# Kernel optimization log

Measured on AMD Instinct MI355X. Metric: run time of the kernel, lower is better.

Reference implementation:

```python
import jax, jax.numpy as jnp
import numpy as np

HEADS = 16
DIM_HEAD = 64
MAX_REL_POS = 16  # temporal_length


def setup_inputs() -> dict:
    key = jax.random.key(0)
    ks = jax.random.split(key, 8)
    B, T, D = 2048, 16, 1024
    inner = HEADS * DIM_HEAD  # 1024
    w = 0.02  # weight init scale for numerical stability
    return {
        "x": jax.random.normal(ks[0], (B, T, D), jnp.float32),
        "Wq": jax.random.normal(ks[1], (inner, D), jnp.float32) * w,
        "Wk": jax.random.normal(ks[2], (inner, D), jnp.float32) * w,
        "Wv": jax.random.normal(ks[3], (inner, D), jnp.float32) * w,
        "Wo": jax.random.normal(ks[4], (D, inner), jnp.float32) * w,
        "bo": jnp.zeros((D,), jnp.float32),
        "rel_k_table": jax.random.normal(ks[5], (2 * MAX_REL_POS + 1, DIM_HEAD), jnp.float32) * w,
        "rel_v_table": jax.random.normal(ks[6], (2 * MAX_REL_POS + 1, DIM_HEAD), jnp.float32) * w,
    }


def reference(x, Wq, Wk, Wv, Wo, bo, rel_k_table, rel_v_table):
    B, T, D = x.shape
    h, dh = HEADS, DIM_HEAD
    scale = dh ** -0.5

    def split_heads(t):  # [B,T,h*dh] -> [B*h,T,dh]
        return t.reshape(B, T, h, dh).transpose(0, 2, 1, 3).reshape(B * h, T, dh)

    q = split_heads(x @ Wq.T)
    k = split_heads(x @ Wk.T)
    v = split_heads(x @ Wv.T)

    sim = jnp.einsum('bid,bjd->bij', q, k) * scale

    # relative-position bias: idx[i,j] = clip(j-i, -L, L) + L
    r = jnp.arange(T)
    idx = jnp.clip(r[None, :] - r[:, None], -MAX_REL_POS, MAX_REL_POS) + MAX_REL_POS
    k2 = rel_k_table[idx]  # [T,T,dh]
    sim = sim + jnp.einsum('btd,tsd->bts', q, k2) * scale

    attn = jax.nn.softmax(sim, axis=-1)
    out = jnp.einsum('bij,bjd->bid', attn, v)
    v2 = rel_v_table[idx]  # [T,T,dh]
    out = out + jnp.einsum('bts,tsd->btd', attn, v2)

    out = out.reshape(B, h, T, dh).transpose(0, 2, 1, 3).reshape(B, T, h * dh)
    return out @ Wo.T + bo
```

## Files before the change

### kernel.cpp

```cpp
#include <hip/hip_runtime.h>

#define HEADS 16
#define DIM_HEAD 64
#define T_SEQ 16
#define D_MODEL 1024
#define MAX_REL 16

typedef _Float16 half8 __attribute__((ext_vector_type(8)));
typedef float f32x4 __attribute__((ext_vector_type(4)));

__global__ __launch_bounds__(256)
void cvt_f32_f16(const float* __restrict__ in, _Float16* __restrict__ out, int n8) {
  int i = blockIdx.x * blockDim.x + threadIdx.x;
  if (i >= n8) return;
  float4 a = ((const float4*)in)[2 * i];
  float4 b = ((const float4*)in)[2 * i + 1];
  half8 h;
  h[0] = (_Float16)a.x; h[1] = (_Float16)a.y;
  h[2] = (_Float16)a.z; h[3] = (_Float16)a.w;
  h[4] = (_Float16)b.x; h[5] = (_Float16)b.y;
  h[6] = (_Float16)b.z; h[7] = (_Float16)b.w;
  ((half8*)out)[i] = h;
}

__device__ __forceinline__ void gload_lds16(const _Float16* g, _Float16* l) {
  __builtin_amdgcn_global_load_lds(
      (const __attribute__((address_space(1))) unsigned int*)(uintptr_t)g,
      (__attribute__((address_space(3))) unsigned int*)(uintptr_t)l, 16, 0, 0);
}

template <bool OUT_F16>
__global__ __launch_bounds__(512, 2)
void gemm256(const _Float16* __restrict__ A, const _Float16* __restrict__ B,
             const float* __restrict__ bias, void* __restrict__ Cv,
             int M, int N, int K) {
  __shared__ _Float16 lds[2][2][2][128][64];
  const int tid = threadIdx.x;
  const int wave = tid >> 6, lane = tid & 63;
  const int wm = wave >> 2, wn = wave & 3;
  const int bm = blockIdx.y, bn = blockIdx.x;
  const int fr = lane & 15;
  const int q4 = lane >> 4;
  const int l3 = lane >> 3;
  const int sl = (lane & 7) ^ l3;

  const _Float16* Ag = A + (size_t)(bm * 256) * K;
  const _Float16* Bg = B + (size_t)(bn * 256) * K;

  f32x4 acc[8][4];
#pragma unroll
  for (int m = 0; m < 8; ++m)
#pragma unroll
    for (int n = 0; n < 4; ++n) acc[m][n] = (f32x4){0.f, 0.f, 0.f, 0.f};

  auto stage_half = [&](int buf, int ab, int half, const _Float16* G, int k0) {
#pragma unroll
    for (int i = 0; i < 2; ++i) {
      int g = wave * 2 + i;
      const _Float16* src =
          G + (size_t)(half * 128 + g * 8 + l3) * K + k0 + sl * 8;
      gload_lds16(src, &lds[buf][ab][half][g * 8][0]);
    }
  };

  auto ldA = [&](int buf, int mf, int ks) {
    unsigned off = (unsigned)((mf * 16 + fr) * 128 + (ks * 4 + q4) * 16) ^
                   (unsigned)((fr & 7) << 4);
    return *(const half8*)((const char*)&lds[buf][0][wm][0][0] + off);
  };
  auto ldB = [&](int buf, int nf, int ks) {
    int rowB = wn * 64 + nf * 16 + fr;
    unsigned off = (unsigned)((rowB & 127) * 128 + (ks * 4 + q4) * 16) ^
                   (unsigned)((fr & 7) << 4);
    return *(const half8*)((const char*)&lds[buf][1][rowB >> 7][0][0] + off);
  };

#pragma unroll
  for (int h = 0; h < 2; ++h) {
    stage_half(0, 0, h, Ag, 0);
    stage_half(0, 1, h, Bg, 0);
  }
  asm volatile("s_waitcnt vmcnt(0)" ::: "memory");
  __builtin_amdgcn_s_barrier();

  const int NT = K >> 6;
  for (int t = 0; t < NT; ++t) {
    const int cur = t & 1, nxt = cur ^ 1;
    const bool pf = (t + 1 < NT);
    const int k1 = (t + 1) << 6;
    half8 bF[4][2];
#pragma unroll
    for (int p = 0; p < 4; ++p) {
      half8 aF[2][2];
#pragma unroll
      for (int i = 0; i < 2; ++i)
#pragma unroll
        for (int ks = 0; ks < 2; ++ks) aF[i][ks] = ldA(cur, p * 2 + i, ks);
      if (p == 0) {
#pragma unroll
        for (int nf = 0; nf < 4; ++nf)
#pragma unroll
          for (int ks = 0; ks < 2; ++ks) bF[nf][ks] = ldB(cur, nf, ks);
      }
      if (pf) {
        if (p < 2) stage_half(nxt, 0, p, Ag, k1);
        else       stage_half(nxt, 1, p - 2, Bg, k1);
      }
      __builtin_amdgcn_s_barrier();
      asm volatile("s_waitcnt lgkmcnt(0)" ::: "memory");
      __builtin_amdgcn_sched_barrier(0);
      __builtin_amdgcn_s_setprio(1);
#pragma unroll
      for (int i = 0; i < 2; ++i)
#pragma unroll
        for (int nf = 0; nf < 4; ++nf)
#pragma unroll
          for (int ks = 0; ks < 2; ++ks)
            acc[p * 2 + i][nf] = __builtin_amdgcn_mfma_f32_16x16x32_f16(
                aF[i][ks], bF[nf][ks], acc[p * 2 + i][nf], 0, 0, 0);
      __builtin_amdgcn_s_setprio(0);
      __builtin_amdgcn_sched_barrier(0);
      if (p == 3) asm volatile("s_waitcnt vmcnt(0)" ::: "memory");
      __builtin_amdgcn_s_barrier();
    }
  }

  const int row_l = q4 * 4;
#pragma unroll
  for (int mf = 0; mf < 8; ++mf) {
#pragma unroll
    for (int nf = 0; nf < 4; ++nf) {
      int col = bn * 256 + wn * 64 + nf * 16 + fr;
#pragma unroll
      for (int r = 0; r < 4; ++r) {
        int row = bm * 256 + wm * 128 + mf * 16 + row_l + r;
        if (OUT_F16) {
          ((_Float16*)Cv)[(size_t)row * N + col] = (_Float16)acc[mf][nf][r];
        } else {
          ((float*)Cv)[(size_t)row * N + col] = acc[mf][nf][r] + bias[col];
        }
      }
    }
  }
}

__global__ __launch_bounds__(256)
void attn_mfma(const _Float16* __restrict__ QKV,
               const float* __restrict__ relk, const float* __restrict__ relv,
               _Float16* __restrict__ O) {
  __shared__ _Float16 RK[32][72];
  __shared__ _Float16 RVt[64][40];
  __shared__ _Float16 PB[4][16][72];
  __shared__ _Float16 VtP[4][64][40];

  const int tid = threadIdx.x;
  const int wave = tid >> 6, lane = tid & 63;

  {
    int m = tid >> 3;
    int d0 = (tid & 7) * 8;
    float4 a = *(const float4*)(relk + m * 64 + d0);
    float4 b = *(const float4*)(relk + m * 64 + d0 + 4);
    half8 hk;
    hk[0] = (_Float16)a.x; hk[1] = (_Float16)a.y;
    hk[2] = (_Float16)a.z; hk[3] = (_Float16)a.w;
    hk[4] = (_Float16)b.x; hk[5] = (_Float16)b.y;
    hk[6] = (_Float16)b.z; hk[7] = (_Float16)b.w;
    *(half8*)&RK[m][d0] = hk;
    float4 c = *(const float4*)(relv + m * 64 + d0);
    float4 d = *(const float4*)(relv + m * 64 + d0 + 4);
    RVt[d0 + 0][m] = (_Float16)c.x; RVt[d0 + 1][m] = (_Float16)c.y;
    RVt[d0 + 2][m] = (_Float16)c.z; RVt[d0 + 3][m] = (_Float16)c.w;
    RVt[d0 + 4][m] = (_Float16)d.x; RVt[d0 + 5][m] = (_Float16)d.y;
    RVt[d0 + 6][m] = (_Float16)d.z; RVt[d0 + 7][m] = (_Float16)d.w;
  }

#pragma unroll
  for (int z = 0; z < 6; ++z) {
    int idx = z * 64 + lane;
    int row = idx / 24, cd = idx % 24;
    *(unsigned int*)&PB[wave][row][16 + 2 * cd] = 0u;
  }
#pragma unroll
  for (int z = 0; z < 8; ++z) {
    int idx = z * 64 + lane;
    int row = idx >> 3, cd = idx & 7;
    *(unsigned int*)&VtP[wave][row][16 + 2 * cd] = 0u;
  }

  const int bh = blockIdx.x * 4 + wave;
  const int b = bh >> 4, h = bh & 15;
  const size_t qbase = (size_t)(b * T_SEQ) * 3072 + h * 64;
  const int fr = lane & 15, fk8 = (lane >> 4) * 8;

  half8 aQ0 = *(const half8*)(QKV + qbase + (size_t)fr * 3072 + fk8);
  half8 aQ1 = *(const half8*)(QKV + qbase + (size_t)fr * 3072 + 32 + fk8);
  half8 bK0 = *(const half8*)(QKV + qbase + 1024 + (size_t)fr * 3072 + fk8);
  half8 bK1 = *(const half8*)(QKV + qbase + 1024 + (size_t)fr * 3072 + 32 + fk8);

  {
    const _Float16* vp = QKV + qbase + 2048 + (size_t)fr * 3072 + (lane >> 4) * 16;
    half8 v0 = *(const half8*)vp;
    half8 v1 = *(const half8*)(vp + 8);
    int d0 = (lane >> 4) * 16;
#pragma unroll
    for (int e = 0; e < 8; ++e) VtP[wave][d0 + e][fr] = v0[e];
#pragma unroll
    for (int e = 0; e < 8; ++e) VtP[wave][d0 + 8 + e][fr] = v1[e];
  }

  __syncthreads();

  f32x4 accS = {0.f, 0.f, 0.f, 0.f};
  accS = __builtin_amdgcn_mfma_f32_16x16x32_f16(aQ0, bK0, accS, 0, 0, 0);
  accS = __builtin_amdgcn_mfma_f32_16x16x32_f16(aQ1, bK1, accS, 0, 0, 0);

  half8 rk0a = *(const half8*)&RK[fr][fk8];
  half8 rk0b = *(const half8*)&RK[fr][32 + fk8];
  half8 rk1a = *(const half8*)&RK[16 + fr][fk8];
  half8 rk1b = *(const half8*)&RK[16 + fr][32 + fk8];
  f32x4 G0 = {0.f, 0.f, 0.f, 0.f}, G1 = {0.f, 0.f, 0.f, 0.f};
  G0 = __builtin_amdgcn_mfma_f32_16x16x32_f16(aQ0, rk0a, G0, 0, 0, 0);
  G0 = __builtin_amdgcn_mfma_f32_16x16x32_f16(aQ1, rk0b, G0, 0, 0, 0);
  G1 = __builtin_amdgcn_mfma_f32_16x16x32_f16(aQ0, rk1a, G1, 0, 0, 0);
  G1 = __builtin_amdgcn_mfma_f32_16x16x32_f16(aQ1, rk1b, G1, 0, 0, 0);

  const int ibase = (lane >> 4) * 4;
#pragma unroll
  for (int r = 0; r < 4; ++r) {
    const int i = ibase + r;
    const int ridx = fr - i + MAX_REL;
    const int src = (lane & 48) | (ridx & 15);
    float g0 = __shfl(G0[r], src);
    float g1 = __shfl(G1[r], src);
    float g = (ridx >= 16) ? g1 : g0;
    float s = (accS[r] + g) * 0.125f;
    float mx = s;
#pragma unroll
    for (int w = 8; w >= 1; w >>= 1) mx = fmaxf(mx, __shfl_xor(mx, w));
    float e = __expf(s - mx);
    float sum = e;
#pragma unroll
    for (int w = 8; w >= 1; w >>= 1) sum += __shfl_xor(sum, w);
    _Float16 ph = (_Float16)(e / sum);
    PB[wave][i][fr] = ph;
    PB[wave][i][32 + (fr - i + MAX_REL)] = ph;
  }

  half8 aP0 = *(const half8*)&PB[wave][fr][fk8];
  half8 aP1 = *(const half8*)&PB[wave][fr][32 + fk8];
  const size_t obase = (size_t)(b * T_SEQ) * D_MODEL + h * 64;
#pragma unroll
  for (int t = 0; t < 4; ++t) {
    half8 bv = *(const half8*)&VtP[wave][t * 16 + fr][fk8];
    half8 br = *(const half8*)&RVt[t * 16 + fr][fk8];
    f32x4 o = {0.f, 0.f, 0.f, 0.f};
    o = __builtin_amdgcn_mfma_f32_16x16x32_f16(aP0, bv, o, 0, 0, 0);
    o = __builtin_amdgcn_mfma_f32_16x16x32_f16(aP1, br, o, 0, 0, 0);
#pragma unroll
    for (int r = 0; r < 4; ++r)
      O[obase + (size_t)(ibase + r) * D_MODEL + t * 16 + fr] = (_Float16)o[r];
  }
}

extern "C" void kernel_launch(void* const* d_in, const int* in_sizes, int n_in,
                              void* d_out, int out_size, void* d_ws, size_t ws_size,
                              hipStream_t stream) {
  const float* x  = (const float*)d_in[0];
  const float* Wq = (const float*)d_in[1];
  const float* Wk = (const float*)d_in[2];
  const float* Wv = (const float*)d_in[3];
  const float* Wo = (const float*)d_in[4];
  const float* bo = (const float*)d_in[5];
  const float* rk = (const float*)d_in[6];
  const float* rv = (const float*)d_in[7];
  float* out = (float*)d_out;

  const int total_rows = 2048 * T_SEQ;
  const size_t wsz = (size_t)D_MODEL * D_MODEL;

  _Float16* Wqkvh = (_Float16*)d_ws;
  _Float16* Woh = Wqkvh + 3 * wsz;
  _Float16* chunk_base = Woh + wsz;

  {
    int n8 = (int)(wsz / 8);
    int blocks = (n8 + 255) / 256;
    cvt_f32_f16<<<blocks, 256, 0, stream>>>(Wq, Wqkvh, n8);
    cvt_f32_f16<<<blocks, 256, 0, stream>>>(Wk, Wqkvh + wsz, n8);
    cvt_f32_f16<<<blocks, 256, 0, stream>>>(Wv, Wqkvh + 2 * wsz, n8);
    cvt_f32_f16<<<blocks, 256, 0, stream>>>(Wo, Woh, n8);
  }

  const size_t per_row_bytes = (size_t)5120 * sizeof(_Float16);
  size_t avail = ws_size - (size_t)4 * wsz * sizeof(_Float16);
  size_t rows_fit = avail / per_row_bytes;
  int rows_c = (rows_fit > (size_t)total_rows) ? total_rows : (int)rows_fit;
  rows_c = (rows_c / 256) * 256;
  if (rows_c < 256) rows_c = 256;

  for (int r0 = 0; r0 < total_rows; r0 += rows_c) {
    int rc = total_rows - r0;
    if (rc > rows_c) rc = rows_c;

    _Float16* xh   = chunk_base;
    _Float16* QKVb = xh + (size_t)rows_c * 1024;
    _Float16* AO   = QKVb + (size_t)rows_c * 3072;

    {
      int n8 = rc * 128;
      cvt_f32_f16<<<(n8 + 255) / 256, 256, 0, stream>>>(
          x + (size_t)r0 * D_MODEL, xh, n8);
    }

    dim3 g1(3072 / 256, rc / 256);
    gemm256<true><<<g1, 512, 0, stream>>>(xh, Wqkvh, nullptr, QKVb,
                                          rc, 3072, 1024);

    attn_mfma<<<rc / 4, 256, 0, stream>>>(QKVb, rk, rv, AO);

    dim3 g2(1024 / 256, rc / 256);
    gemm256<false><<<g2, 512, 0, stream>>>(AO, Woh, bo, out + (size_t)r0 * D_MODEL,
                                           rc, 1024, 1024);
  }
}
```

Measured before the change: 417.3 us.

## Remap GEMM workgroups per XCD and front-load next-tile staging

The GEMM now launches a 1D grid and remaps each block ID so that consecutive tiles land on the same XCD, which keeps neighbouring output tiles sharing A/B data inside one L2. Global-to-LDS prefetch of the next K tile also moves earlier: all A halves are issued in the first sub-step and all B halves in the second, instead of spreading them over four sub-steps. The remap is meant to raise L2 hit rates. Issuing the loads earlier gives more time to hide latency, but may bunch memory traffic together and contend with LDS reads.

```diff
diff --git a/kernel.cpp b/kernel.cpp
--- a/kernel.cpp
+++ b/kernel.cpp
@@ -38,7 +38,16 @@
   const int tid = threadIdx.x;
   const int wave = tid >> 6, lane = tid & 63;
   const int wm = wave >> 2, wn = wave & 3;
-  const int bm = blockIdx.y, bn = blockIdx.x;
+
+  const int GN = N >> 8;
+  const int nwg = gridDim.x;
+  const int q = nwg >> 3, r = nwg & 7;
+  {
+  }
+  const int xcd = blockIdx.x & 7, pos = blockIdx.x >> 3;
+  const int wgid = (xcd < r ? xcd * (q + 1) : r * (q + 1) + (xcd - r) * q) + pos;
+  const int bm = wgid / GN, bn = wgid % GN;
+
   const int fr = lane & 15;
   const int q4 = lane >> 4;
   const int l3 = lane >> 3;
@@ -103,8 +112,13 @@
           for (int ks = 0; ks < 2; ++ks) bF[nf][ks] = ldB(cur, nf, ks);
       }
       if (pf) {
-        if (p < 2) stage_half(nxt, 0, p, Ag, k1);
-        else       stage_half(nxt, 1, p - 2, Bg, k1);
+        if (p == 0) {
+          stage_half(nxt, 0, 0, Ag, k1);
+          stage_half(nxt, 0, 1, Ag, k1);
+        } else if (p == 1) {
+          stage_half(nxt, 1, 0, Bg, k1);
+          stage_half(nxt, 1, 1, Bg, k1);
+        }
       }
       __builtin_amdgcn_s_barrier();
       asm volatile("s_waitcnt lgkmcnt(0)" ::: "memory");
@@ -132,12 +146,12 @@
     for (int nf = 0; nf < 4; ++nf) {
       int col = bn * 256 + wn * 64 + nf * 16 + fr;
 #pragma unroll
-      for (int r = 0; r < 4; ++r) {
-        int row = bm * 256 + wm * 128 + mf * 16 + row_l + r;
+      for (int r4 = 0; r4 < 4; ++r4) {
+        int row = bm * 256 + wm * 128 + mf * 16 + row_l + r4;
         if (OUT_F16) {
-          ((_Float16*)Cv)[(size_t)row * N + col] = (_Float16)acc[mf][nf][r];
+          ((_Float16*)Cv)[(size_t)row * N + col] = (_Float16)acc[mf][nf][r4];
         } else {
-          ((float*)Cv)[(size_t)row * N + col] = acc[mf][nf][r] + bias[col];
+          ((float*)Cv)[(size_t)row * N + col] = acc[mf][nf][r4] + bias[col];
         }
       }
     }
@@ -313,14 +327,12 @@
           x + (size_t)r0 * D_MODEL, xh, n8);
     }
 
-    dim3 g1(3072 / 256, rc / 256);
-    gemm256<true><<<g1, 512, 0, stream>>>(xh, Wqkvh, nullptr, QKVb,
-                                          rc, 3072, 1024);
+    gemm256<true><<<(3072 / 256) * (rc / 256), 512, 0, stream>>>(
+        xh, Wqkvh, nullptr, QKVb, rc, 3072, 1024);
 
     attn_mfma<<<rc / 4, 256, 0, stream>>>(QKVb, rk, rv, AO);
 
-    dim3 g2(1024 / 256, rc / 256);
-    gemm256<false><<<g2, 512, 0, stream>>>(AO, Woh, bo, out + (size_t)r0 * D_MODEL,
-                                           rc, 1024, 1024);
-  }
-}
+    gemm256<false><<<(1024 / 256) * (rc / 256), 512, 0, stream>>>(
+        AO, Woh, bo, out + (size_t)r0 * D_MODEL, rc, 1024, 1024);
+  }
+}
```

Result: no change. 414.6 us (-0.6%).
